# Kernel optimization log

Measured on AMD Instinct MI355X. Metric: run time of the kernel, lower is better.

Reference implementation:

```python
import jax, jax.numpy as jnp
import numpy as np

PI = jnp.pi


def _spow(t, p):
    # t >= 0; safe t**p with value 0 (and zero grad) at t == 0
    tt = jnp.where(t > 0, t, 1.0)
    return jnp.where(t > 0, tt ** p, 0.0)


def _wavelets(t, f, fm, pm, em, fo, ph):
    # t: [L]; f: [S,1] -> returns [S, L] bank of wavelets (one per scale)
    sigma = jnp.maximum(fm / (2.0 * PI * f), 1e-6)        # [S,1]
    br = jnp.cos(2.0 * PI * f * t)                        # [S,L]
    bi = jnp.sin(2.0 * PI * f * t)
    # real_part: + pm0*br - c^2 (t/sig)^fo0 br pm1 + ... alternating, c = 2..7
    real = br * pm[0]
    sign = -1.0
    for j in range(6):
        c = j + 2.0
        real = real + sign * (_spow(t, fo[j]) * c / sigma ** fo[j] * c) * br * pm[j + 1]
        sign = -sign
    # imag_part: same pattern with fo6..fo11, pm8..pm13; j==9 term has the
    # anomalous parenthesization from the source: t**fo*5/(sigma**fo*5)
    imag = bi * pm[7]
    sign = -1.0
    for j in range(6, 12):
        c = j - 4.0
        if j == 9:
            term = (_spow(t, fo[j]) * 5.0 / (sigma ** fo[j] * 5.0)) * bi * pm[j + 2]
        else:
            term = (_spow(t, fo[j]) * c / sigma ** fo[j] * c) * bi * pm[j + 2]
        imag = imag + sign * term
        sign = -sign
    gauss = em[0] * jnp.exp(-t ** 2 / (2.0 * sigma ** 2))  # [S,L]
    rw = real * gauss
    iw = imag * gauss
    amp = rw + iw
    samp = amp / jnp.linalg.norm(amp, axis=-1, keepdims=True)
    phase = jnp.arctan2(iw, rw)
    w = (samp * jnp.sin(phase) * ph[0]) * (samp * jnp.cos(phase) * ph[1]) \
        * (samp * jnp.sinc(phase / PI) * ph[2])
    return w


def reference(x, scales, f_mod, poly_mod, exp_mod, frac_order, phase_mod, i):
    B, C = x.shape[0], x.shape[1]
    xf = x.reshape(B, C, -1)                              # [B,C,L]
    L = xf.shape[-1]
    S = scales.shape[0]
    t = jnp.arange(L, dtype=x.dtype)
    f = (1.0 / scales)[:, None]                           # [S,1]
    W = _wavelets(t, f, f_mod[i], poly_mod[i], exp_mod[i], frac_order[i],
                  phase_mod[i])                            # [S,L] kernels, K = L
    # torch F.conv1d(padding='same', groups=C*S) = cross-correlation with
    # left pad (K-1)//2. Computed exactly via zero-padded FFT linear conv.
    K = L
    Nfft = 2 * L                                          # >= L + K - 1, no aliasing
    Xf = jnp.fft.rfft(xf, n=Nfft, axis=-1)                # [B,C,F]
    Wf = jnp.fft.rfft(W[:, ::-1], n=Nfft, axis=-1)        # [S,F] (corr = conv w/ flip)
    y = jnp.fft.irfft(Xf[:, :, None, :] * Wf[None, None], n=Nfft, axis=-1)  # [B,C,S,2L]
    left = (K - 1) // 2
    off = K - 1 - left
    y = y[..., off:off + L]                               # [B,C,S,L]
    # torch channel layout: out[:, j] = corr(x[:, j % C], wavelet[j % S])
    j = jnp.arange(C * S)
    return y[:, j % C, j % S, :]                          # [B, C*S, L]


def setup_inputs() -> dict:
    key = jax.random.key(0)
    ks = jax.random.split(key, 6)
    B, C, H, Wd = 16, 16, 64, 64
    S, NSTEPS = 16, 10
    x = jax.random.normal(ks[0], (B, C, H, Wd), dtype=jnp.float32)
    scales = jnp.linspace(1.0, 32.0, S, dtype=jnp.float32)
    f_mod = 1.0 + 0.02 * jax.random.normal(ks[1], (NSTEPS,), dtype=jnp.float32)
    poly_mod = 1.0 + 0.02 * jax.random.normal(ks[2], (NSTEPS, 14), dtype=jnp.float32)
    exp_mod = 1.0 + 0.02 * jax.random.normal(ks[3], (NSTEPS, 1), dtype=jnp.float32)
    frac_order = 1.0 + 0.02 * jax.random.normal(ks[4], (NSTEPS, 12), dtype=jnp.float32)
    phase_mod = 1.0 + 0.02 * jax.random.normal(ks[5], (NSTEPS, 3), dtype=jnp.float32)
    return {"x": x, "scales": scales, "f_mod": f_mod, "poly_mod": poly_mod,
            "exp_mod": exp_mod, "frac_order": frac_order,
            "phase_mod": phase_mod, "i": 3}
```

## Files before the change

kernel.cpp:

```cpp
#include <hip/hip_runtime.h>
#include <math.h>

#define QMAX 128
#define ZCUT 1920
#define XPAD 127
#define XLEN 2176
#define XS_SZ 2304

typedef float vfloat4 __attribute__((ext_vector_type(4)));

__global__ __launch_bounds__(256) void conv_diag(const float* __restrict__ x,
                                                 const float* __restrict__ scales,
                                                 const float* __restrict__ f_mod,
                                                 const float* __restrict__ poly_mod,
                                                 const float* __restrict__ exp_mod,
                                                 const float* __restrict__ frac_order,
                                                 const float* __restrict__ phase_mod,
                                                 const int* __restrict__ istep,
                                                 float* __restrict__ out) {
    __shared__ __attribute__((aligned(16))) float xs[XS_SZ];
    __shared__ __attribute__((aligned(16))) float Wl[QMAX];
    __shared__ float wsum[2];

    const int bk = blockIdx.x;
    const int b = bk >> 4;
    const int k = bk & 15;
    const int tid = threadIdx.x;

    const float* xrow = x + (size_t)bk * 4096;
    for (int li = tid; li < XS_SZ; li += 256) {
        xs[li] = (li >= XPAD && li < XPAD + XLEN) ? xrow[li - XPAD] : 0.0f;
    }

    float amp = 0.0f, rw = 0.0f, iw = 0.0f;
    if (tid < QMAX) {
        const int i = istep[0];
        const float PI2 = 6.28318530717958647692f;
        const float f = 1.0f / scales[k];
        const float fm = f_mod[i];
        const float* pm = poly_mod + i * 14;
        const float em0 = exp_mod[i];
        const float* fo = frac_order + i * 12;

        const float sigma = fmaxf(fm / (PI2 * f), 1e-6f);
        const float tf = (float)tid;
        const float arg = PI2 * f * tf;
        const float br = cosf(arg);
        const float bi = sinf(arg);

        float rp = pm[0];
        float sign = -1.0f;
        for (int j = 0; j < 6; ++j) {
            float c = (float)(j + 2);
            float sp = (tf > 0.0f) ? powf(tf, fo[j]) : 0.0f;
            float term = sp * c / powf(sigma, fo[j]) * c * pm[j + 1];
            rp += sign * term;
            sign = -sign;
        }
        float ipoly = pm[7];
        sign = -1.0f;
        for (int j = 6; j < 12; ++j) {
            float sp = (tf > 0.0f) ? powf(tf, fo[j]) : 0.0f;
            float term;
            if (j == 9) {
                term = sp * 5.0f / (powf(sigma, fo[j]) * 5.0f) * pm[j + 2];
            } else {
                float c = (float)(j - 4);
                term = sp * c / powf(sigma, fo[j]) * c * pm[j + 2];
            }
            ipoly += sign * term;
            sign = -sign;
        }

        const float gauss = em0 * expf(-tf * tf / (2.0f * sigma * sigma));
        rw = br * rp * gauss;
        iw = bi * ipoly * gauss;
        amp = rw + iw;

        float sq = amp * amp;
        #pragma unroll
        for (int off = 32; off > 0; off >>= 1) sq += __shfl_xor(sq, off, 64);
        if ((tid & 63) == 0) wsum[tid >> 6] = sq;
    }
    __syncthreads();

    if (tid < QMAX) {
        const int i = istep[0];
        const float* ph = phase_mod + i * 3;
        const float norm = sqrtf(wsum[0] + wsum[1]);
        const float samp = amp / norm;
        const float phase = atan2f(iw, rw);
        const float sphi = sinf(phase);
        const float cphi = cosf(phase);
        const float snc = (phase != 0.0f) ? (sphi / phase) : 1.0f;
        Wl[tid] = (samp * sphi * ph[0]) * (samp * cphi * ph[1]) * (samp * snc * ph[2]);
    }
    __syncthreads();

    float* orow = out + ((size_t)b * 256 + k) * 4096;
    #pragma unroll
    for (int v = 0; v < 4; ++v) {
        const int p = 4 * (tid + 256 * v);
        float4 val = make_float4(0.0f, 0.0f, 0.0f, 0.0f);
        if (p >= ZCUT) {
            float acc[4] = {0.0f, 0.0f, 0.0f, 0.0f};
            const int base = p - 1920;
            for (int q = 0; q < QMAX; q += 4) {
                float4 w4 = *(const float4*)&Wl[q];
                float4 x0 = *(const float4*)&xs[base + q];
                float4 x1 = *(const float4*)&xs[base + q + 4];
                float win[8] = {x0.x, x0.y, x0.z, x0.w,
                                x1.x, x1.y, x1.z, x1.w};
                float wv[4] = {w4.x, w4.y, w4.z, w4.w};
                #pragma unroll
                for (int j = 0; j < 4; ++j) {
                    #pragma unroll
                    for (int r = 0; r < 4; ++r) {
                        acc[r] = fmaf(win[r + j], wv[j], acc[r]);
                    }
                }
            }
            val = make_float4(acc[0], acc[1], acc[2], acc[3]);
        }
        *(float4*)&orow[p] = val;
    }
}

__global__ __launch_bounds__(256) void replicate_rows(float* __restrict__ out) {
    const int blk = blockIdx.x;
    const int b = blk / 240;
    const int j = 16 + (blk - b * 240);
    const int k = j & 15;
    const float* __restrict__ src = out + ((size_t)b * 256 + k) * 4096;
    float* __restrict__ dst = out + ((size_t)b * 256 + j) * 4096;
    const int tid = threadIdx.x;
    #pragma unroll
    for (int v = 0; v < 4; ++v) {
        const int e = 4 * (tid + 256 * v);
        vfloat4 val = *(const vfloat4*)&src[e];
        __builtin_nontemporal_store(val, (vfloat4*)&dst[e]);
    }
}

extern "C" void kernel_launch(void* const* d_in, const int* in_sizes, int n_in,
                              void* d_out, int out_size, void* d_ws, size_t ws_size,
                              hipStream_t stream) {
    const float* x          = (const float*)d_in[0];
    const float* scales     = (const float*)d_in[1];
    const float* f_mod      = (const float*)d_in[2];
    const float* poly_mod   = (const float*)d_in[3];
    const float* exp_mod    = (const float*)d_in[4];
    const float* frac_order = (const float*)d_in[5];
    const float* phase_mod  = (const float*)d_in[6];
    const int*   istep      = (const int*)d_in[7];
    float* out = (float*)d_out;

    conv_diag<<<dim3(256), dim3(256), 0, stream>>>(
        x, scales, f_mod, poly_mod, exp_mod, frac_order, phase_mod, istep, out);

    replicate_rows<<<dim3(3840), dim3(256), 0, stream>>>(out);
}
```

Measured before the change: 35.76 us.

## Stage conv rows in workspace, double block size, replicate all rows with zero prefix

The conv kernel now writes its 256 diagonal rows to a compact workspace buffer and runs 512 threads per block, two float4 outputs per thread, so more waves share the convolution work. The inner loop carries the previous float4 of x forward, cutting shared-memory loads per step from two to one. The replicate kernel now writes all 4096 output rows from the workspace and stores zeros directly for the prefix below ZCUT, skipping those reads. This removes the read-after-write dependency on the output rows but adds a second write of the 256 source rows into the output.

Measured after the change: 35.54 us. No clear change (-0.6%).

```diff
diff --git a/kernel.cpp b/kernel.cpp
--- a/kernel.cpp
+++ b/kernel.cpp
@@ -9,7 +9,7 @@
 
 typedef float vfloat4 __attribute__((ext_vector_type(4)));
 
-__global__ __launch_bounds__(256) void conv_diag(const float* __restrict__ x,
+__global__ __launch_bounds__(512) void conv_diag(const float* __restrict__ x,
                                                  const float* __restrict__ scales,
                                                  const float* __restrict__ f_mod,
                                                  const float* __restrict__ poly_mod,
@@ -17,18 +17,17 @@
                                                  const float* __restrict__ frac_order,
                                                  const float* __restrict__ phase_mod,
                                                  const int* __restrict__ istep,
-                                                 float* __restrict__ out) {
+                                                 float* __restrict__ ws) {
     __shared__ __attribute__((aligned(16))) float xs[XS_SZ];
     __shared__ __attribute__((aligned(16))) float Wl[QMAX];
     __shared__ float wsum[2];
 
     const int bk = blockIdx.x;
-    const int b = bk >> 4;
     const int k = bk & 15;
     const int tid = threadIdx.x;
 
     const float* xrow = x + (size_t)bk * 4096;
-    for (int li = tid; li < XS_SZ; li += 256) {
+    for (int li = tid; li < XS_SZ; li += 512) {
         xs[li] = (li >= XPAD && li < XPAD + XLEN) ? xrow[li - XPAD] : 0.0f;
     }
 
@@ -53,8 +52,7 @@
         for (int j = 0; j < 6; ++j) {
             float c = (float)(j + 2);
             float sp = (tf > 0.0f) ? powf(tf, fo[j]) : 0.0f;
-            float term = sp * c / powf(sigma, fo[j]) * c * pm[j + 1];
-            rp += sign * term;
+            rp += sign * (sp * c / powf(sigma, fo[j]) * c * pm[j + 1]);
             sign = -sign;
         }
         float ipoly = pm[7];
@@ -97,20 +95,21 @@
     }
     __syncthreads();
 
-    float* orow = out + ((size_t)b * 256 + k) * 4096;
+    float* wrow = ws + (size_t)bk * 4096;
     #pragma unroll
-    for (int v = 0; v < 4; ++v) {
-        const int p = 4 * (tid + 256 * v);
+    for (int v = 0; v < 2; ++v) {
+        const int fidx = tid + 512 * v;
+        const int p = 4 * fidx;
         float4 val = make_float4(0.0f, 0.0f, 0.0f, 0.0f);
         if (p >= ZCUT) {
             float acc[4] = {0.0f, 0.0f, 0.0f, 0.0f};
             const int base = p - 1920;
+            float4 xcur = *(const float4*)&xs[base];
             for (int q = 0; q < QMAX; q += 4) {
                 float4 w4 = *(const float4*)&Wl[q];
-                float4 x0 = *(const float4*)&xs[base + q];
-                float4 x1 = *(const float4*)&xs[base + q + 4];
-                float win[8] = {x0.x, x0.y, x0.z, x0.w,
-                                x1.x, x1.y, x1.z, x1.w};
+                float4 xnxt = *(const float4*)&xs[base + q + 4];
+                float win[8] = {xcur.x, xcur.y, xcur.z, xcur.w,
+                                xnxt.x, xnxt.y, xnxt.z, xnxt.w};
                 float wv[4] = {w4.x, w4.y, w4.z, w4.w};
                 #pragma unroll
                 for (int j = 0; j < 4; ++j) {
@@ -119,25 +118,28 @@
                         acc[r] = fmaf(win[r + j], wv[j], acc[r]);
                     }
                 }
+                xcur = xnxt;
             }
             val = make_float4(acc[0], acc[1], acc[2], acc[3]);
         }
-        *(float4*)&orow[p] = val;
+        *(float4*)&wrow[p] = val;
     }
 }
 
-__global__ __launch_bounds__(256) void replicate_rows(float* __restrict__ out) {
-    const int blk = blockIdx.x;
-    const int b = blk / 240;
-    const int j = 16 + (blk - b * 240);
+__global__ __launch_bounds__(256) void replicate_rows(const float* __restrict__ ws,
+                                                      float* __restrict__ out) {
+    const int m = blockIdx.x;
+    const int b = m >> 8;
+    const int j = m & 255;
     const int k = j & 15;
-    const float* __restrict__ src = out + ((size_t)b * 256 + k) * 4096;
-    float* __restrict__ dst = out + ((size_t)b * 256 + j) * 4096;
+    const float* __restrict__ src = ws + ((size_t)b * 16 + k) * 4096;
+    float* __restrict__ dst = out + (size_t)m * 4096;
     const int tid = threadIdx.x;
     #pragma unroll
     for (int v = 0; v < 4; ++v) {
         const int e = 4 * (tid + 256 * v);
-        vfloat4 val = *(const vfloat4*)&src[e];
+        vfloat4 val = (e >= ZCUT) ? *(const vfloat4*)&src[e]
+                                  : (vfloat4){0.0f, 0.0f, 0.0f, 0.0f};
         __builtin_nontemporal_store(val, (vfloat4*)&dst[e]);
     }
 }
@@ -154,9 +156,10 @@
     const float* phase_mod  = (const float*)d_in[6];
     const int*   istep      = (const int*)d_in[7];
     float* out = (float*)d_out;
+    float* wsd = (float*)d_ws;
 
-    conv_diag<<<dim3(256), dim3(256), 0, stream>>>(
-        x, scales, f_mod, poly_mod, exp_mod, frac_order, phase_mod, istep, out);
+    conv_diag<<<dim3(256), dim3(512), 0, stream>>>(
+        x, scales, f_mod, poly_mod, exp_mod, frac_order, phase_mod, istep, wsd);
 
-    replicate_rows<<<dim3(3840), dim3(256), 0, stream>>>(out);
+    replicate_rows<<<dim3(4096), dim3(256), 0, stream>>>(wsd, out);
 }
```
